# Performance work log

Measured on AMD Instinct MI355X. Metric: run time of the kernel, lower is better.

The kernel has to match this reference:

```python
import jax, jax.numpy as jnp
import numpy as np
from math import factorial

# ---- module config (matches init_kwargs) ----
K_MAX_L = [256, 192, 128, 64]
L_MAX = len(K_MAX_L) - 1
PADDED = [2 * ((l + 1) // 2) for l in range(L_MAX + 1)]  # [0, 2, 2, 4]
N_SAMPLES = 32768

# ---- real Clebsch-Gordan coefficients (numpy, float64, done once at import) ----

def _cg_coeff(j1, m1, j2, m2, J, M):
    # Racah formula for complex-basis CG coefficient <j1 m1 j2 m2 | J M>
    if m1 + m2 != M:
        return 0.0
    pref = (2 * J + 1) * factorial(j1 + j2 - J) * factorial(j1 - j2 + J) \
        * factorial(-j1 + j2 + J) / factorial(j1 + j2 + J + 1)
    pref *= factorial(J + M) * factorial(J - M) * factorial(j1 - m1) \
        * factorial(j1 + m1) * factorial(j2 - m2) * factorial(j2 + m2)
    kmin = max(0, j2 - J - m1, j1 + m2 - J)
    kmax = min(j1 + j2 - J, j1 - m1, j2 + m2)
    s = 0.0
    for k in range(kmin, kmax + 1):
        s += (-1) ** k / (factorial(k) * factorial(j1 + j2 - J - k)
                          * factorial(j1 - m1 - k) * factorial(j2 + m2 - k)
                          * factorial(J - j2 + m1 + k) * factorial(J - j1 - m2 + k))
    return np.sqrt(pref) * s


def _cg_complex(j1, j2, J):
    cg = np.zeros((2 * j1 + 1, 2 * j2 + 1, 2 * J + 1))
    for m1 in range(-j1, j1 + 1):
        for m2 in range(-j2, j2 + 1):
            M = m1 + m2
            if abs(M) <= J:
                cg[m1 + j1, m2 + j2, M + J] = _cg_coeff(j1, m1, j2, m2, J, M)
    return cg


def _real2complex(L):
    # maps real spherical-harmonic components to complex ones (unitary)
    res = np.zeros((2 * L + 1, 2 * L + 1), dtype=np.complex128)
    isq2 = 1.0 / np.sqrt(2.0)
    for m in range(-L, L + 1):
        if m < 0:
            res[L - m, L + m] = isq2 * 1j * (-1) ** m
            res[L + m, L + m] = -isq2 * 1j
        elif m == 0:
            res[L, L] = 1.0
        else:
            res[L - m, L + m] = isq2
            res[L + m, L + m] = isq2 * (-1) ** m
    return res


def _cg_real(l1, l2, L):
    ccg = _cg_complex(l1, l2, L).astype(np.complex128)
    tmp = np.einsum('ma,nb,mnM->abM', _real2complex(l1), _real2complex(l2), ccg)
    out = np.einsum('abM,kM->abk', tmp, np.conjugate(_real2complex(L)).T)
    return np.real(out) if (l1 + l2 + L) % 2 == 0 else np.imag(out)


def _build_U(padded_l):
    half = padded_l // 2
    blocks = [_cg_real(half, half, L) for L in range(padded_l + 1)]
    U = np.concatenate(blocks, axis=2).reshape((padded_l + 1) ** 2, (padded_l + 1) ** 2)
    assert np.allclose(U @ U.T, np.eye((padded_l + 1) ** 2), atol=1e-10)
    return U

_U_DICT = {pl: jnp.asarray(_build_U(pl), dtype=jnp.float32) for pl in sorted(set(PADDED))}

# ---- forward (pure jnp) ----

def _split_bands(features):
    # band l holds channels [k_max_l[l+1]:k_max_l[l]) of all features lp<=l
    bands = []
    for l in range(L_MAX + 1):
        lo = K_MAX_L[l + 1] if l < L_MAX else 0
        hi = K_MAX_L[l]
        bands.append([features[lp][:, :, lo:hi] for lp in range(l + 1)])
    return bands


def _uncouple(feats, U, pl):
    n, w = feats[0].shape[0], feats[0].shape[-1]
    if len(feats) < pl + 1:  # pad missing top-l block with zeros (odd l case)
        feats = feats + [jnp.zeros((n, 2 * pl + 1, w), feats[0].dtype)]
    stacked = jnp.concatenate(feats, axis=1)               # (n, (pl+1)^2, w)
    unc = jnp.einsum('MN,nNw->nMw', U, stacked)
    return unc.reshape(n, pl + 1, pl + 1, w)


def _couple(x, U, pl):
    n, w = x.shape[0], x.shape[-1]
    flat = x.reshape(n, (pl + 1) ** 2, w)
    coup = jnp.einsum('NM,nNw->nMw', U, flat)              # U.T contraction
    sizes = np.cumsum([2 * L + 1 for L in range(pl + 1)])[:-1]
    return jnp.split(coup, sizes, axis=1)


def _tensor_product(f1, f2):
    b1, b2 = _split_bands(f1), _split_bands(f2)
    coupled = []
    for l in range(L_MAX + 1):
        pl = PADDED[l]
        U = _U_DICT[pl]
        u1 = _uncouple(b1[l], U, pl)                       # (n, pl+1, pl+1, w)
        u2 = _uncouple(b2[l], U, pl)
        comb = jnp.einsum('nijw,njkw->nikw', u1, u2)       # per-channel matmul
        coupled.append(_couple(comb, U, pl))
    return tuple(
        jnp.concatenate([coupled[lp][l] for lp in range(l, L_MAX + 1)], axis=-1)
        for l in range(L_MAX + 1)
    )


def setup_inputs() -> dict:
    key = jax.random.key(0)
    keys = jax.random.split(key, 8)
    out = {}
    i = 0
    for tag in ('f1', 'f2'):
        for l in range(L_MAX + 1):
            out[f'{tag}_{l}'] = jax.random.normal(
                keys[i], (N_SAMPLES, 2 * l + 1, K_MAX_L[l]), dtype=jnp.float32)
            i += 1
    return out


def reference(f1_0, f1_1, f1_2, f1_3, f2_0, f2_1, f2_2, f2_3):
    return _tensor_product([f1_0, f1_1, f1_2, f1_3], [f2_0, f2_1, f2_2, f2_3])
```

## Files before the change

kernel.cpp:

```cpp
#include <hip/hip_runtime.h>

#define NS 32768
#define OUT1_BASE (NS * 256)
#define OUT2_BASE (OUT1_BASE + NS * 576)
#define OUT3_BASE (OUT2_BASE + NS * 640)

namespace cgc {

constexpr double hfact(int n) { double r = 1.0; for (int i = 2; i <= n; ++i) r *= (double)i; return r; }

constexpr double csqrt(double a) {
    if (a <= 0.0) return 0.0;
    double x = a > 1.0 ? a : 1.0;
    for (int i = 0; i < 64; ++i) x = 0.5 * (x + a / x);
    return x;
}

constexpr double cg_coeff(int j1, int m1, int j2, int m2, int J, int M) {
    if (m1 + m2 != M) return 0.0;
    double pref = (2.0 * J + 1.0) * hfact(j1 + j2 - J) * hfact(j1 - j2 + J)
                * hfact(-j1 + j2 + J) / hfact(j1 + j2 + J + 1);
    pref *= hfact(J + M) * hfact(J - M) * hfact(j1 - m1) * hfact(j1 + m1)
          * hfact(j2 - m2) * hfact(j2 + m2);
    int kmin = 0;
    if (j2 - J - m1 > kmin) kmin = j2 - J - m1;
    if (j1 + m2 - J > kmin) kmin = j1 + m2 - J;
    int kmax = j1 + j2 - J;
    if (j1 - m1 < kmax) kmax = j1 - m1;
    if (j2 + m2 < kmax) kmax = j2 + m2;
    double s = 0.0;
    for (int k = kmin; k <= kmax; ++k) {
        double d = hfact(k) * hfact(j1 + j2 - J - k) * hfact(j1 - m1 - k)
                 * hfact(j2 + m2 - k) * hfact(J - j2 + m1 + k) * hfact(J - j1 - m2 + k);
        s += ((k & 1) ? -1.0 : 1.0) / d;
    }
    return csqrt(pref) * s;
}

struct C2 { double re; double im; };
constexpr C2 cmul(C2 a, C2 b) { return { a.re * b.re - a.im * b.im, a.re * b.im + a.im * b.re }; }
constexpr C2 cadd(C2 a, C2 b) { return { a.re + b.re, a.im + b.im }; }
constexpr C2 cscale(C2 a, double s) { return { a.re * s, a.im * s }; }
constexpr C2 conjc(C2 a) { return { a.re, -a.im }; }

struct R2C { C2 r[81]; };

constexpr R2C real2complex(int L) {
    R2C R{};
    int D = 2 * L + 1;
    double isq2 = 0.70710678118654752440084436210485;
    isq2 = 1.0 / csqrt(2.0);
    for (int m = -L; m <= L; ++m) {
        double sgn = (m & 1) ? -1.0 : 1.0;
        if (m < 0) {
            R.r[(L - m) * D + (L + m)] = { 0.0, isq2 * sgn };
            R.r[(L + m) * D + (L + m)] = { 0.0, -isq2 };
        } else if (m == 0) {
            R.r[L * D + L] = { 1.0, 0.0 };
        } else {
            R.r[(L - m) * D + (L + m)] = { isq2, 0.0 };
            R.r[(L + m) * D + (L + m)] = { isq2 * sgn, 0.0 };
        }
    }
    return R;
}

struct Blk { double v[225]; };

constexpr Blk cg_real(int l1, int l2, int L) {
    Blk out{};
    int D1 = 2 * l1 + 1, D2 = 2 * l2 + 1, DL = 2 * L + 1;
    double ccg[225] = {};
    for (int m1 = -l1; m1 <= l1; ++m1)
        for (int m2 = -l2; m2 <= l2; ++m2) {
            int M = m1 + m2;
            if (M >= -L && M <= L)
                ccg[((m1 + l1) * D2 + (m2 + l2)) * DL + (M + L)] = cg_coeff(l1, m1, l2, m2, L, M);
        }
    R2C R1 = real2complex(l1);
    R2C R2 = real2complex(l2);
    R2C RL = real2complex(L);
    bool even = ((l1 + l2 + L) % 2) == 0;
    for (int a = 0; a < D1; ++a)
        for (int b = 0; b < D2; ++b) {
            C2 tmp[9] = {};
            for (int M = 0; M < DL; ++M) {
                C2 s = { 0.0, 0.0 };
                for (int m = 0; m < D1; ++m)
                    for (int nn = 0; nn < D2; ++nn) {
                        double cc = ccg[(m * D2 + nn) * DL + M];
                        if (cc != 0.0)
                            s = cadd(s, cscale(cmul(R1.r[m * D1 + a], R2.r[nn * D2 + b]), cc));
                    }
                tmp[M] = s;
            }
            for (int k = 0; k < DL; ++k) {
                C2 s = { 0.0, 0.0 };
                for (int M = 0; M < DL; ++M)
                    s = cadd(s, cmul(tmp[M], conjc(RL.r[M * DL + k])));
                out.v[(a * D2 + b) * DL + k] = even ? s.re : s.im;
            }
        }
    return out;
}

constexpr Blk B2_0 = cg_real(1, 1, 0);
constexpr Blk B2_1 = cg_real(1, 1, 1);
constexpr Blk B2_2 = cg_real(1, 1, 2);
constexpr Blk B4_0 = cg_real(2, 2, 0);
constexpr Blk B4_1 = cg_real(2, 2, 1);
constexpr Blk B4_2 = cg_real(2, 2, 2);
constexpr Blk B4_3 = cg_real(2, 2, 3);
constexpr Blk B4_4 = cg_real(2, 2, 4);

struct U9T  { float u[81];  };
struct U25T { float u[625]; };

constexpr U9T build_U9() {
    U9T U{};
    const Blk* bl[3] = { &B2_0, &B2_1, &B2_2 };
    int off = 0;
    for (int L = 0; L <= 2; ++L) {
        int DL = 2 * L + 1;
        for (int a = 0; a < 3; ++a)
            for (int b = 0; b < 3; ++b)
                for (int k = 0; k < DL; ++k)
                    U.u[(a * 3 + b) * 9 + (off + k)] = (float)bl[L]->v[(a * 3 + b) * DL + k];
        off += DL;
    }
    return U;
}

constexpr U25T build_U25() {
    U25T U{};
    const Blk* bl[5] = { &B4_0, &B4_1, &B4_2, &B4_3, &B4_4 };
    int off = 0;
    for (int L = 0; L <= 4; ++L) {
        int DL = 2 * L + 1;
        for (int a = 0; a < 5; ++a)
            for (int b = 0; b < 5; ++b)
                for (int k = 0; k < DL; ++k)
                    U.u[(a * 5 + b) * 25 + (off + k)] = (float)bl[L]->v[(a * 5 + b) * DL + k];
        off += DL;
    }
    return U;
}

constexpr U9T  U9c  = build_U9();
constexpr U25T U25c = build_U25();

}


__global__ __launch_bounds__(256) void tp_fused_kernel(
    const float* __restrict__ f1_0, const float* __restrict__ f1_1,
    const float* __restrict__ f1_2, const float* __restrict__ f1_3,
    const float* __restrict__ f2_0, const float* __restrict__ f2_1,
    const float* __restrict__ f2_2, const float* __restrict__ f2_3,
    float* __restrict__ out)
{
    using namespace cgc;
    const int t = blockIdx.x * 256 + threadIdx.x;
    const int n = t >> 6, c = t & 63;
    const int r0 = n * 256, r1 = n * 576, r2 = n * 640, r3 = n * 448;

    out[r0 + c] = f1_0[r0 + 192 + c] * f2_0[r0 + 192 + c];

    {
        const int ch = 128 + c;
        float x1[4], x2[4];
        x1[0] = f1_0[r0 + ch];
        x2[0] = f2_0[r0 + ch];
#pragma unroll
        for (int m = 0; m < 3; ++m) {
            x1[1 + m] = f1_1[r1 + m * 192 + ch];
            x2[1 + m] = f2_1[r1 + m * 192 + ch];
        }
        float A[9], B[9];
#pragma unroll
        for (int M = 0; M < 9; ++M) {
            float sa = 0.f, sb = 0.f;
#pragma unroll
            for (int N = 0; N < 4; ++N)
                if (U9c.u[M * 9 + N] != 0.0f) {
                    sa += U9c.u[M * 9 + N] * x1[N];
                    sb += U9c.u[M * 9 + N] * x2[N];
                }
            A[M] = sa; B[M] = sb;
        }
        float C[9];
#pragma unroll
        for (int i = 0; i < 3; ++i)
#pragma unroll
            for (int k = 0; k < 3; ++k) {
                float s = 0.f;
#pragma unroll
                for (int j = 0; j < 3; ++j) s += A[i * 3 + j] * B[j * 3 + k];
                C[i * 3 + k] = s;
            }
        float y[4];
#pragma unroll
        for (int M = 0; M < 4; ++M) {
            float s = 0.f;
#pragma unroll
            for (int N = 0; N < 9; ++N)
                if (U9c.u[N * 9 + M] != 0.0f) s += U9c.u[N * 9 + M] * C[N];
            y[M] = s;
        }
        out[r0 + 64 + c] = y[0];
#pragma unroll
        for (int m = 0; m < 3; ++m)
            out[OUT1_BASE + r1 + m * 192 + c] = y[1 + m];
    }

    {
        const int ch = 64 + c;
        float x1[9], x2[9];
        x1[0] = f1_0[r0 + ch];
        x2[0] = f2_0[r0 + ch];
#pragma unroll
        for (int m = 0; m < 3; ++m) {
            x1[1 + m] = f1_1[r1 + m * 192 + ch];
            x2[1 + m] = f2_1[r1 + m * 192 + ch];
        }
#pragma unroll
        for (int m = 0; m < 5; ++m) {
            x1[4 + m] = f1_2[r2 + m * 128 + ch];
            x2[4 + m] = f2_2[r2 + m * 128 + ch];
        }
        float A[9], B[9];
#pragma unroll
        for (int M = 0; M < 9; ++M) {
            float sa = 0.f, sb = 0.f;
#pragma unroll
            for (int N = 0; N < 9; ++N)
                if (U9c.u[M * 9 + N] != 0.0f) {
                    sa += U9c.u[M * 9 + N] * x1[N];
                    sb += U9c.u[M * 9 + N] * x2[N];
                }
            A[M] = sa; B[M] = sb;
        }
        float C[9];
#pragma unroll
        for (int i = 0; i < 3; ++i)
#pragma unroll
            for (int k = 0; k < 3; ++k) {
                float s = 0.f;
#pragma unroll
                for (int j = 0; j < 3; ++j) s += A[i * 3 + j] * B[j * 3 + k];
                C[i * 3 + k] = s;
            }
        float y[9];
#pragma unroll
        for (int M = 0; M < 9; ++M) {
            float s = 0.f;
#pragma unroll
            for (int N = 0; N < 9; ++N)
                if (U9c.u[N * 9 + M] != 0.0f) s += U9c.u[N * 9 + M] * C[N];
            y[M] = s;
        }
        out[r0 + 128 + c] = y[0];
#pragma unroll
        for (int m = 0; m < 3; ++m)
            out[OUT1_BASE + r1 + m * 192 + 64 + c] = y[1 + m];
#pragma unroll
        for (int m = 0; m < 5; ++m)
            out[OUT2_BASE + r2 + m * 128 + c] = y[4 + m];
    }

    {
        float x1[16], x2[16];
        x1[0] = f1_0[r0 + c];
        x2[0] = f2_0[r0 + c];
#pragma unroll
        for (int m = 0; m < 3; ++m) {
            x1[1 + m] = f1_1[r1 + m * 192 + c];
            x2[1 + m] = f2_1[r1 + m * 192 + c];
        }
#pragma unroll
        for (int m = 0; m < 5; ++m) {
            x1[4 + m] = f1_2[r2 + m * 128 + c];
            x2[4 + m] = f2_2[r2 + m * 128 + c];
        }
#pragma unroll
        for (int m = 0; m < 7; ++m) {
            x1[9 + m] = f1_3[r3 + m * 64 + c];
            x2[9 + m] = f2_3[r3 + m * 64 + c];
        }
        float A[25], B[25];
#pragma unroll
        for (int M = 0; M < 25; ++M) {
            float sa = 0.f, sb = 0.f;
#pragma unroll
            for (int N = 0; N < 16; ++N)
                if (U25c.u[M * 25 + N] != 0.0f) {
                    sa += U25c.u[M * 25 + N] * x1[N];
                    sb += U25c.u[M * 25 + N] * x2[N];
                }
            A[M] = sa; B[M] = sb;
        }
        float C[25];
#pragma unroll
        for (int i = 0; i < 5; ++i)
#pragma unroll
            for (int k = 0; k < 5; ++k) {
                float s = 0.f;
#pragma unroll
                for (int j = 0; j < 5; ++j) s += A[i * 5 + j] * B[j * 5 + k];
                C[i * 5 + k] = s;
            }
        float y[16];
#pragma unroll
        for (int M = 0; M < 16; ++M) {
            float s = 0.f;
#pragma unroll
            for (int N = 0; N < 25; ++N)
                if (U25c.u[N * 25 + M] != 0.0f) s += U25c.u[N * 25 + M] * C[N];
            y[M] = s;
        }
        out[r0 + 192 + c] = y[0];
#pragma unroll
        for (int m = 0; m < 3; ++m)
            out[OUT1_BASE + r1 + m * 192 + 128 + c] = y[1 + m];
#pragma unroll
        for (int m = 0; m < 5; ++m)
            out[OUT2_BASE + r2 + m * 128 + 64 + c] = y[4 + m];
#pragma unroll
        for (int m = 0; m < 7; ++m)
            out[OUT3_BASE + r3 + m * 64 + c] = y[9 + m];
    }
}

extern "C" void kernel_launch(void* const* d_in, const int* in_sizes, int n_in,
                              void* d_out, int out_size, void* d_ws, size_t ws_size,
                              hipStream_t stream)
{
    const float* f1_0 = (const float*)d_in[0];
    const float* f1_1 = (const float*)d_in[1];
    const float* f1_2 = (const float*)d_in[2];
    const float* f1_3 = (const float*)d_in[3];
    const float* f2_0 = (const float*)d_in[4];
    const float* f2_1 = (const float*)d_in[5];
    const float* f2_2 = (const float*)d_in[6];
    const float* f2_3 = (const float*)d_in[7];
    float* out = (float*)d_out;

    dim3 blk(256);
    dim3 grid(NS / 4);

    tp_fused_kernel<<<grid, blk, 0, stream>>>(f1_0, f1_1, f1_2, f1_3,
                                              f2_0, f2_1, f2_2, f2_3, out);
}
```

Before: 143.0 us.

## Stage inputs and outputs through LDS with vectorized float4 loads and nontemporal stores

Loads all input bands for four samples into shared memory using 128-bit vector loads, computes the tensor product from LDS, then stages outputs back in LDS and writes them with vectorized nontemporal stores. The aim is wider, fully contiguous global transactions and less cache pollution from outputs. In exchange it uses about 60KB of LDS per block and adds two extra barriers, which reduces occupancy and latency hiding.

```diff
diff --git a/kernel.cpp b/kernel.cpp
--- a/kernel.cpp
+++ b/kernel.cpp
@@ -4,6 +4,8 @@
 #define OUT1_BASE (NS * 256)
 #define OUT2_BASE (OUT1_BASE + NS * 576)
 #define OUT3_BASE (OUT2_BASE + NS * 640)
+
+typedef float f4 __attribute__((ext_vector_type(4)));
 
 namespace cgc {
 
@@ -48,8 +50,7 @@
 constexpr R2C real2complex(int L) {
     R2C R{};
     int D = 2 * L + 1;
-    double isq2 = 0.70710678118654752440084436210485;
-    isq2 = 1.0 / csqrt(2.0);
+    double isq2 = 1.0 / csqrt(2.0);
     for (int m = -L; m <= L; ++m) {
         double sgn = (m & 1) ? -1.0 : 1.0;
         if (m < 0) {
@@ -152,7 +153,33 @@
 }
 
 
-__global__ __launch_bounds__(256) void tp_fused_kernel(
+#define L4_F1_0 0
+#define L4_F1_1 256
+#define L4_F1_2 832
+#define L4_F1_3 1472
+#define L4_F2_0 1920
+#define L4_F2_1 2176
+#define L4_F2_2 2752
+#define L4_F2_3 3392
+#define L4_TOT  3840
+#define LF_F1_0 0
+#define LF_F1_1 1024
+#define LF_F1_2 3328
+#define LF_F1_3 5888
+#define LF_F2_0 7680
+#define LF_F2_1 8704
+#define LF_F2_2 11008
+#define LF_F2_3 13568
+#define LF_O0 0
+#define LF_O1 1024
+#define LF_O2 3328
+#define LF_O3 5888
+#define L4_O0 0
+#define L4_O1 256
+#define L4_O2 832
+#define L4_O3 1472
+
+__global__ __launch_bounds__(256) void tp_lds_kernel(
     const float* __restrict__ f1_0, const float* __restrict__ f1_1,
     const float* __restrict__ f1_2, const float* __restrict__ f1_3,
     const float* __restrict__ f2_0, const float* __restrict__ f2_1,
@@ -160,21 +187,68 @@
     float* __restrict__ out)
 {
     using namespace cgc;
-    const int t = blockIdx.x * 256 + threadIdx.x;
-    const int n = t >> 6, c = t & 63;
-    const int r0 = n * 256, r1 = n * 576, r2 = n * 640, r3 = n * 448;
-
-    out[r0 + c] = f1_0[r0 + 192 + c] * f2_0[r0 + 192 + c];
+    __shared__ f4 lds4[L4_TOT];
+    float* lds = (float*)lds4;
+
+    const int tid = threadIdx.x;
+    const int n0 = blockIdx.x * 4;
+
+    {
+        const f4* g10 = (const f4*)f1_0 + n0 * 64;
+        const f4* g11 = (const f4*)f1_1 + n0 * 144;
+        const f4* g12 = (const f4*)f1_2 + n0 * 160;
+        const f4* g13 = (const f4*)f1_3 + n0 * 112;
+        const f4* g20 = (const f4*)f2_0 + n0 * 64;
+        const f4* g21 = (const f4*)f2_1 + n0 * 144;
+        const f4* g22 = (const f4*)f2_2 + n0 * 160;
+        const f4* g23 = (const f4*)f2_3 + n0 * 112;
+
+        lds4[L4_F1_0 + tid]       = g10[tid];
+        lds4[L4_F1_1 + tid]       = g11[tid];
+        lds4[L4_F1_1 + 256 + tid] = g11[256 + tid];
+        lds4[L4_F1_2 + tid]       = g12[tid];
+        lds4[L4_F1_2 + 256 + tid] = g12[256 + tid];
+        lds4[L4_F1_3 + tid]       = g13[tid];
+        lds4[L4_F2_0 + tid]       = g20[tid];
+        lds4[L4_F2_1 + tid]       = g21[tid];
+        lds4[L4_F2_1 + 256 + tid] = g21[256 + tid];
+        lds4[L4_F2_2 + tid]       = g22[tid];
+        lds4[L4_F2_2 + 256 + tid] = g22[256 + tid];
+        lds4[L4_F2_3 + tid]       = g23[tid];
+        if (tid < 64) {
+            lds4[L4_F1_1 + 512 + tid] = g11[512 + tid];
+            lds4[L4_F2_1 + 512 + tid] = g21[512 + tid];
+        }
+        if (tid < 128) {
+            lds4[L4_F1_2 + 512 + tid] = g12[512 + tid];
+            lds4[L4_F2_2 + 512 + tid] = g22[512 + tid];
+        }
+        if (tid < 192) {
+            lds4[L4_F1_3 + 256 + tid] = g13[256 + tid];
+            lds4[L4_F2_3 + 256 + tid] = g23[256 + tid];
+        }
+    }
+    __syncthreads();
+
+    const int s = tid >> 6, c = tid & 63;
+    const int b0 = s * 256, b1 = s * 576, b2 = s * 640, b3 = s * 448;
+
+    float y0;
+    float y1[4];
+    float y2[9];
+    float y3[16];
+
+    y0 = lds[LF_F1_0 + b0 + 192 + c] * lds[LF_F2_0 + b0 + 192 + c];
 
     {
         const int ch = 128 + c;
         float x1[4], x2[4];
-        x1[0] = f1_0[r0 + ch];
-        x2[0] = f2_0[r0 + ch];
+        x1[0] = lds[LF_F1_0 + b0 + ch];
+        x2[0] = lds[LF_F2_0 + b0 + ch];
 #pragma unroll
         for (int m = 0; m < 3; ++m) {
-            x1[1 + m] = f1_1[r1 + m * 192 + ch];
-            x2[1 + m] = f2_1[r1 + m * 192 + ch];
+            x1[1 + m] = lds[LF_F1_1 + b1 + m * 192 + ch];
+            x2[1 + m] = lds[LF_F2_1 + b1 + m * 192 + ch];
         }
         float A[9], B[9];
 #pragma unroll
@@ -193,40 +267,35 @@
         for (int i = 0; i < 3; ++i)
 #pragma unroll
             for (int k = 0; k < 3; ++k) {
-                float s = 0.f;
-#pragma unroll
-                for (int j = 0; j < 3; ++j) s += A[i * 3 + j] * B[j * 3 + k];
-                C[i * 3 + k] = s;
+                float sC = 0.f;
+#pragma unroll
+                for (int j = 0; j < 3; ++j) sC += A[i * 3 + j] * B[j * 3 + k];
+                C[i * 3 + k] = sC;
             }
-        float y[4];
 #pragma unroll
         for (int M = 0; M < 4; ++M) {
-            float s = 0.f;
+            float sY = 0.f;
 #pragma unroll
             for (int N = 0; N < 9; ++N)
-                if (U9c.u[N * 9 + M] != 0.0f) s += U9c.u[N * 9 + M] * C[N];
-            y[M] = s;
-        }
-        out[r0 + 64 + c] = y[0];
-#pragma unroll
-        for (int m = 0; m < 3; ++m)
-            out[OUT1_BASE + r1 + m * 192 + c] = y[1 + m];
+                if (U9c.u[N * 9 + M] != 0.0f) sY += U9c.u[N * 9 + M] * C[N];
+            y1[M] = sY;
+        }
     }
 
     {
         const int ch = 64 + c;
         float x1[9], x2[9];
-        x1[0] = f1_0[r0 + ch];
-        x2[0] = f2_0[r0 + ch];
+        x1[0] = lds[LF_F1_0 + b0 + ch];
+        x2[0] = lds[LF_F2_0 + b0 + ch];
 #pragma unroll
         for (int m = 0; m < 3; ++m) {
-            x1[1 + m] = f1_1[r1 + m * 192 + ch];
-            x2[1 + m] = f2_1[r1 + m * 192 + ch];
+            x1[1 + m] = lds[LF_F1_1 + b1 + m * 192 + ch];
+            x2[1 + m] = lds[LF_F2_1 + b1 + m * 192 + ch];
         }
 #pragma unroll
         for (int m = 0; m < 5; ++m) {
-            x1[4 + m] = f1_2[r2 + m * 128 + ch];
-            x2[4 + m] = f2_2[r2 + m * 128 + ch];
+            x1[4 + m] = lds[LF_F1_2 + b2 + m * 128 + ch];
+            x2[4 + m] = lds[LF_F2_2 + b2 + m * 128 + ch];
         }
         float A[9], B[9];
 #pragma unroll
@@ -245,47 +314,39 @@
         for (int i = 0; i < 3; ++i)
 #pragma unroll
             for (int k = 0; k < 3; ++k) {
-                float s = 0.f;
-#pragma unroll
-                for (int j = 0; j < 3; ++j) s += A[i * 3 + j] * B[j * 3 + k];
-                C[i * 3 + k] = s;
+                float sC = 0.f;
+#pragma unroll
+                for (int j = 0; j < 3; ++j) sC += A[i * 3 + j] * B[j * 3 + k];
+                C[i * 3 + k] = sC;
             }
-        float y[9];
 #pragma unroll
         for (int M = 0; M < 9; ++M) {
-            float s = 0.f;
+            float sY = 0.f;
 #pragma unroll
             for (int N = 0; N < 9; ++N)
-                if (U9c.u[N * 9 + M] != 0.0f) s += U9c.u[N * 9 + M] * C[N];
-            y[M] = s;
-        }
-        out[r0 + 128 + c] = y[0];
-#pragma unroll
-        for (int m = 0; m < 3; ++m)
-            out[OUT1_BASE + r1 + m * 192 + 64 + c] = y[1 + m];
-#pragma unroll
-        for (int m = 0; m < 5; ++m)
-            out[OUT2_BASE + r2 + m * 128 + c] = y[4 + m];
+                if (U9c.u[N * 9 + M] != 0.0f) sY += U9c.u[N * 9 + M] * C[N];
+            y2[M] = sY;
+        }
     }
 
     {
         float x1[16], x2[16];
-        x1[0] = f1_0[r0 + c];
-        x2[0] = f2_0[r0 + c];
+        x1[0] = lds[LF_F1_0 + b0 + c];
+        x2[0] = lds[LF_F2_0 + b0 + c];
 #pragma unroll
         for (int m = 0; m < 3; ++m) {
-            x1[1 + m] = f1_1[r1 + m * 192 + c];
-            x2[1 + m] = f2_1[r1 + m * 192 + c];
+            x1[1 + m] = lds[LF_F1_1 + b1 + m * 192 + c];
+            x2[1 + m] = lds[LF_F2_1 + b1 + m * 192 + c];
         }
 #pragma unroll
         for (int m = 0; m < 5; ++m) {
-            x1[4 + m] = f1_2[r2 + m * 128 + c];
-            x2[4 + m] = f2_2[r2 + m * 128 + c];
+            x1[4 + m] = lds[LF_F1_2 + b2 + m * 128 + c];
+            x2[4 + m] = lds[LF_F2_2 + b2 + m * 128 + c];
         }
 #pragma unroll
         for (int m = 0; m < 7; ++m) {
-            x1[9 + m] = f1_3[r3 + m * 64 + c];
-            x2[9 + m] = f2_3[r3 + m * 64 + c];
+            x1[9 + m] = lds[LF_F1_3 + b3 + m * 64 + c];
+            x2[9 + m] = lds[LF_F2_3 + b3 + m * 64 + c];
         }
         float A[25], B[25];
 #pragma unroll
@@ -304,30 +365,62 @@
         for (int i = 0; i < 5; ++i)
 #pragma unroll
             for (int k = 0; k < 5; ++k) {
-                float s = 0.f;
-#pragma unroll
-                for (int j = 0; j < 5; ++j) s += A[i * 5 + j] * B[j * 5 + k];
-                C[i * 5 + k] = s;
+                float sC = 0.f;
+#pragma unroll
+                for (int j = 0; j < 5; ++j) sC += A[i * 5 + j] * B[j * 5 + k];
+                C[i * 5 + k] = sC;
             }
-        float y[16];
 #pragma unroll
         for (int M = 0; M < 16; ++M) {
-            float s = 0.f;
+            float sY = 0.f;
 #pragma unroll
             for (int N = 0; N < 25; ++N)
-                if (U25c.u[N * 25 + M] != 0.0f) s += U25c.u[N * 25 + M] * C[N];
-            y[M] = s;
-        }
-        out[r0 + 192 + c] = y[0];
-#pragma unroll
-        for (int m = 0; m < 3; ++m)
-            out[OUT1_BASE + r1 + m * 192 + 128 + c] = y[1 + m];
-#pragma unroll
-        for (int m = 0; m < 5; ++m)
-            out[OUT2_BASE + r2 + m * 128 + 64 + c] = y[4 + m];
-#pragma unroll
-        for (int m = 0; m < 7; ++m)
-            out[OUT3_BASE + r3 + m * 64 + c] = y[9 + m];
+                if (U25c.u[N * 25 + M] != 0.0f) sY += U25c.u[N * 25 + M] * C[N];
+            y3[M] = sY;
+        }
+    }
+
+    __syncthreads();
+
+    lds[LF_O0 + b0 + c]        = y0;
+    lds[LF_O0 + b0 + 64 + c]   = y1[0];
+    lds[LF_O0 + b0 + 128 + c]  = y2[0];
+    lds[LF_O0 + b0 + 192 + c]  = y3[0];
+#pragma unroll
+    for (int m = 0; m < 3; ++m) {
+        lds[LF_O1 + b1 + m * 192 + c]        = y1[1 + m];
+        lds[LF_O1 + b1 + m * 192 + 64 + c]   = y2[1 + m];
+        lds[LF_O1 + b1 + m * 192 + 128 + c]  = y3[1 + m];
+    }
+#pragma unroll
+    for (int m = 0; m < 5; ++m) {
+        lds[LF_O2 + b2 + m * 128 + c]       = y2[4 + m];
+        lds[LF_O2 + b2 + m * 128 + 64 + c]  = y3[4 + m];
+    }
+#pragma unroll
+    for (int m = 0; m < 7; ++m)
+        lds[LF_O3 + b3 + m * 64 + c] = y3[9 + m];
+
+    __syncthreads();
+
+    {
+        f4* o0 = (f4*)out + n0 * 64;
+        f4* o1 = (f4*)out + 2097152 + n0 * 144;
+        f4* o2 = (f4*)out + 6815744 + n0 * 160;
+        f4* o3 = (f4*)out + 12058624 + n0 * 112;
+
+        __builtin_nontemporal_store(lds4[L4_O0 + tid],       &o0[tid]);
+        __builtin_nontemporal_store(lds4[L4_O1 + tid],       &o1[tid]);
+        __builtin_nontemporal_store(lds4[L4_O1 + 256 + tid], &o1[256 + tid]);
+        __builtin_nontemporal_store(lds4[L4_O2 + tid],       &o2[tid]);
+        __builtin_nontemporal_store(lds4[L4_O2 + 256 + tid], &o2[256 + tid]);
+        __builtin_nontemporal_store(lds4[L4_O3 + tid],       &o3[tid]);
+        if (tid < 64)
+            __builtin_nontemporal_store(lds4[L4_O1 + 512 + tid], &o1[512 + tid]);
+        if (tid < 128)
+            __builtin_nontemporal_store(lds4[L4_O2 + 512 + tid], &o2[512 + tid]);
+        if (tid < 192)
+            __builtin_nontemporal_store(lds4[L4_O3 + 256 + tid], &o3[256 + tid]);
     }
 }
 
@@ -348,6 +441,6 @@
     dim3 blk(256);
     dim3 grid(NS / 4);
 
-    tp_fused_kernel<<<grid, blk, 0, stream>>>(f1_0, f1_1, f1_2, f1_3,
-                                              f2_0, f2_1, f2_2, f2_3, out);
-}
+    tp_lds_kernel<<<grid, blk, 0, stream>>>(f1_0, f1_1, f1_2, f1_3,
+                                            f2_0, f2_1, f2_2, f2_3, out);
+}
```

After: 147.2 us. 1.03x slower.
